# Optimization experiments

Measured on AMD Instinct MI355X. Metric: run time of the kernel, lower is better.

Reference implementation:

```python
import jax, jax.numpy as jnp
import numpy as np
import math

D, H, F = 1024, 16, 4096
DH = D // H
EPS_LN = 1e-5


def _layernorm(x, scale, bias):
    mu = jnp.mean(x, axis=-1, keepdims=True)
    var = jnp.mean(jnp.square(x - mu), axis=-1, keepdims=True)
    return (x - mu) * jax.lax.rsqrt(var + EPS_LN) * scale + bias


def setup_inputs() -> dict:
    key = jax.random.key(0)
    ks = jax.random.split(key, 16)
    B, T = 2, 2048
    src = jax.random.normal(ks[0], (B, T, D), dtype=jnp.float32)
    attn_mask = jax.random.randint(ks[1], (T, T), 0, 2) == 1  # bool [T,S], True = masked
    xavier = lambda k, shp: jax.random.uniform(k, shp, jnp.float32, -1.0, 1.0) * math.sqrt(6.0 / (shp[0] + shp[1]))
    return {
        "src": src, "attn_mask": attn_mask,
        "q_w": xavier(ks[2], (D, D)), "q_b": jnp.zeros((D,), jnp.float32),
        "k_w": xavier(ks[3], (D, D)), "k_b": jnp.zeros((D,), jnp.float32),
        "v_w": xavier(ks[4], (D, D)), "v_b": jnp.zeros((D,), jnp.float32),
        "o_w": xavier(ks[5], (D, D)), "o_b": jnp.zeros((D,), jnp.float32),
        "l1_w": xavier(ks[6], (F, D)), "l1_b": jnp.zeros((F,), jnp.float32),
        "l2_w": xavier(ks[7], (D, F)), "l2_b": jnp.zeros((D,), jnp.float32),
        "n1_s": jnp.ones((D,), jnp.float32), "n1_b": jnp.zeros((D,), jnp.float32),
        "n2_s": jnp.ones((D,), jnp.float32), "n2_b": jnp.zeros((D,), jnp.float32),
        "alpha_attn": jax.random.normal(ks[8], (), jnp.float32) * 0.1,
        "alpha_ff": jax.random.normal(ks[9], (), jnp.float32) * 0.1,
    }


def reference(src, attn_mask, q_w, q_b, k_w, k_b, v_w, v_b, o_w, o_b,
              l1_w, l1_b, l2_w, l2_b, n1_s, n1_b, n2_s, n2_b,
              alpha_attn, alpha_ff):
    B, T, _ = src.shape
    # --- self-attention block (post-norm layer, dropout=0 => identity) ---
    q = (src @ q_w.T + q_b).reshape(B, T, H, DH).transpose(0, 2, 1, 3)  # [B,H,T,DH]
    k = (src @ k_w.T + k_b).reshape(B, T, H, DH).transpose(0, 2, 1, 3)
    v = (src @ v_w.T + v_b).reshape(B, T, H, DH).transpose(0, 2, 1, 3)
    scores = jnp.einsum('bhtd,bhsd->bhts', q, k) / math.sqrt(DH)  # [B,H,T,S]
    scores = jnp.where(attn_mask[None, None, :, :], -jnp.inf, scores)
    probs = jax.nn.softmax(scores + 1e-9, axis=-1)
    probs = jnp.where(jnp.isinf(scores), 0.0, probs)  # zero where masked (custom semantics)
    attn = jnp.einsum('bhts,bhsd->bhtd', probs, v).transpose(0, 2, 1, 3).reshape(B, T, D)
    attn = attn @ o_w.T + o_b
    x = _layernorm(src + alpha_attn * attn, n1_s, n1_b)
    # --- FFN block ---
    ff = jax.nn.relu(x @ l1_w.T + l1_b) @ l2_w.T + l2_b
    x = _layernorm(x + alpha_ff * ff, n2_s, n2_b)
    return x
```

## Files before the change

### kernel.cpp

```cpp
#include <hip/hip_runtime.h>
#include <math.h>

#define Dm 1024
#define Hh 16
#define DHd 64
#define Ff 4096
#define Tt 2048
#define Bb 2

#define ATT_C2 0.18033688011112042f

typedef __bf16 bf16_8 __attribute__((ext_vector_type(8)));
typedef __bf16 bf16x2 __attribute__((ext_vector_type(2)));
typedef __bf16 bf16x4 __attribute__((ext_vector_type(4)));
typedef float  f32x4  __attribute__((ext_vector_type(4)));
typedef float  f32x16 __attribute__((ext_vector_type(16)));
typedef unsigned int u32x4 __attribute__((ext_vector_type(4)));

__device__ __forceinline__ unsigned short f2bf(float f) {
    unsigned int u = __float_as_uint(f);
    unsigned int r = (u + 0x7fffu + ((u >> 16) & 1u)) >> 16;
    return (unsigned short)r;
}

__device__ __forceinline__ bf16x2 pkbf(float a, float b) {
#if __has_builtin(__builtin_amdgcn_cvt_pk_bf16_f32)
    return __builtin_amdgcn_cvt_pk_bf16_f32(a, b);
#else
    bf16x2 r; r[0] = (__bf16)a; r[1] = (__bf16)b; return r;
#endif
}
__device__ __forceinline__ bf16x4 pkbf4(float a, float b, float c, float d) {
    bf16x2 lo = pkbf(a, b), hi = pkbf(c, d);
    return __builtin_shufflevector(lo, hi, 0, 1, 2, 3);
}

__device__ __forceinline__ void plswap32(unsigned &a, unsigned &b) {
#if __has_builtin(__builtin_amdgcn_permlane32_swap)
    auto r = __builtin_amdgcn_permlane32_swap((int)a, (int)b, false, false);
    a = (unsigned)r[0]; b = (unsigned)r[1];
#else
    asm volatile("v_permlane32_swap_b32 %0, %1" : "+v"(a), "+v"(b));
#endif
}

__device__ __forceinline__ void gld_lds16(const void* g, void* l) {
    __builtin_amdgcn_global_load_lds(
        (const __attribute__((address_space(1))) void*)g,
        (__attribute__((address_space(3))) void*)l,
        16, 0, 0);
}

__global__ __launch_bounds__(256) void preprocess_kernel(
    const float* __restrict__ q_w, const float* __restrict__ k_w,
    const float* __restrict__ v_w, const float* __restrict__ o_w,
    const float* __restrict__ l1_w, const float* __restrict__ l2_w,
    const float* __restrict__ src, const int* __restrict__ mask,
    const float* __restrict__ q_b, const float* __restrict__ k_b,
    unsigned short* __restrict__ qkw, unsigned short* __restrict__ vw16,
    unsigned short* __restrict__ ow,  unsigned short* __restrict__ l1w,
    unsigned short* __restrict__ l2w, unsigned short* __restrict__ srcb,
    unsigned* __restrict__ mbit, float* __restrict__ qkb)
{
    const int bid = blockIdx.x;
    const int tid = threadIdx.x;
    if (bid < 16384) {
        int i = bid * 256 + tid;
        const float* sp; unsigned short* dp; int off;
        if (i < 1048576) {
            if (i < 262144)      { sp = q_w; dp = qkw;           off = i; }
            else if (i < 524288) { sp = k_w; dp = qkw + 1048576; off = i - 262144; }
            else if (i < 786432) { sp = v_w; dp = vw16;          off = i - 524288; }
            else                 { sp = o_w; dp = ow;            off = i - 786432; }
        } else if (i < 2097152)  { sp = l1_w; dp = l1w;          off = i - 1048576; }
        else if (i < 3145728)    { sp = l2_w; dp = l2w;          off = i - 2097152; }
        else                     { sp = src;  dp = srcb;         off = i - 3145728; }
        float4 v = ((const float4*)sp)[off];
        ((bf16x4*)dp)[off] = pkbf4(v.x, v.y, v.z, v.w);
    } else if (bid < 16896) {
        int w = (bid - 16384) * 256 + tid;
        const int* p = mask + (size_t)w * 32;
        unsigned bits = 0;
        #pragma unroll
        for (int j = 0; j < 8; ++j) {
            int4 v = ((const int4*)p)[j];
            bits |= (v.x != 0 ? 1u : 0u) << (j * 4 + 0);
            bits |= (v.y != 0 ? 1u : 0u) << (j * 4 + 1);
            bits |= (v.z != 0 ? 1u : 0u) << (j * 4 + 2);
            bits |= (v.w != 0 ? 1u : 0u) << (j * 4 + 3);
        }
        mbit[w] = bits;
    } else {
        int i = (bid - 16896) * 256 + tid;
        qkb[i] = (i < 1024) ? q_b[i] : k_b[i - 1024];
    }
}

template<int RELU, int BF16OUT>
__global__ __launch_bounds__(256) void gemm_bf16_kernel(
    const unsigned short* __restrict__ A, const unsigned short* __restrict__ W,
    const float* __restrict__ bias, void* __restrict__ C, void* __restrict__ C2,
    int M, int N, int K, int ldc, int ksub)
{
    __shared__ __bf16 As[128][64];
    __shared__ __bf16 Bs[128][64];
    const int tid  = threadIdx.x;
    const int lane = tid & 63;
    const int wave = tid >> 6;
    const int m0 = blockIdx.y * 128;
    const int n0 = blockIdx.x * 128;
    const int lr8 = lane >> 3;
    const int gch = (lane & 7) ^ lr8;
    const int wm = (wave & 1) * 64;
    const int wn = (wave >> 1) * 64;
    const int quad = lane >> 4;
    const int lm = lane & 15;
    const int z  = blockIdx.z;
    const int kstart = z * ksub;
    void* Cz = (z == 0) ? C : C2;

    f32x4 acc[4][4];
    #pragma unroll
    for (int i = 0; i < 4; i++)
        #pragma unroll
        for (int j = 0; j < 4; j++) {
            acc[i][j][0] = 0.f; acc[i][j][1] = 0.f;
            acc[i][j][2] = 0.f; acc[i][j][3] = 0.f;
        }

    for (int k0 = kstart; k0 < kstart + ksub; k0 += 64) {
        __syncthreads();
        #pragma unroll
        for (int i = 0; i < 4; i++) {
            int seg = wave * 4 + i;
            int r = seg * 8 + lr8;
            gld_lds16(A + (size_t)(m0 + r) * K + k0 + gch * 8, &As[seg * 8][0]);
            gld_lds16(W + (size_t)(n0 + r) * K + k0 + gch * 8, &Bs[seg * 8][0]);
        }
        __syncthreads();
        #pragma unroll
        for (int kh = 0; kh < 2; kh++) {
            bf16_8 af[4], bfr[4];
            #pragma unroll
            for (int t = 0; t < 4; t++) {
                int ch = (kh * 4 + quad) ^ (lm & 7);
                af[t]  = *(const bf16_8*)&As[wm + t * 16 + lm][ch * 8];
                bfr[t] = *(const bf16_8*)&Bs[wn + t * 16 + lm][ch * 8];
            }
            #pragma unroll
            for (int i = 0; i < 4; i++)
                #pragma unroll
                for (int j = 0; j < 4; j++)
                    acc[i][j] = __builtin_amdgcn_mfma_f32_16x16x32_bf16(
                        af[i], bfr[j], acc[i][j], 0, 0, 0);
        }
    }

    float bvc[4];
    #pragma unroll
    for (int j = 0; j < 4; j++)
        bvc[j] = (z == 0) ? bias[n0 + wn + j * 16 + lm] : 0.f;

    #pragma unroll
    for (int i = 0; i < 4; i++)
        #pragma unroll
        for (int j = 0; j < 4; j++) {
            int col = n0 + wn + j * 16 + lm;
            #pragma unroll
            for (int r = 0; r < 4; r++) {
                int row = m0 + wm + i * 16 + quad * 4 + r;
                float v = acc[i][j][r] + bvc[j];
                if (RELU) v = fmaxf(v, 0.f);
                if (BF16OUT)
                    ((unsigned short*)Cz)[(size_t)row * ldc + col] = f2bf(v);
                else
                    ((float*)Cz)[(size_t)row * ldc + col] = v;
            }
        }
}

__global__ __launch_bounds__(256, 2) void gemm_ffn1_kernel(
    const unsigned short* __restrict__ A, const unsigned short* __restrict__ W,
    const float* __restrict__ bias, unsigned short* __restrict__ C)
{
    __shared__ __bf16 As[256][64];
    __shared__ __bf16 Bs[128][64];
    const int tid  = threadIdx.x;
    const int lane = tid & 63;
    const int wave = tid >> 6;
    const int m0 = blockIdx.y * 256;
    const int n0 = blockIdx.x * 128;
    const int lr8 = lane >> 3;
    const int gch = (lane & 7) ^ lr8;
    const int quad = lane >> 4;
    const int lm = lane & 15;

    f32x4 acc[4][8];
    #pragma unroll
    for (int i = 0; i < 4; i++)
        #pragma unroll
        for (int j = 0; j < 8; j++) {
            acc[i][j][0] = 0.f; acc[i][j][1] = 0.f;
            acc[i][j][2] = 0.f; acc[i][j][3] = 0.f;
        }

    for (int k0 = 0; k0 < 1024; k0 += 64) {
        __syncthreads();
        #pragma unroll
        for (int i = 0; i < 8; i++) {
            int seg = wave * 8 + i;
            int r = seg * 8 + lr8;
            gld_lds16(A + (size_t)(m0 + r) * 1024 + k0 + gch * 8, &As[seg * 8][0]);
        }
        #pragma unroll
        for (int i = 0; i < 4; i++) {
            int seg = wave * 4 + i;
            int r = seg * 8 + lr8;
            gld_lds16(W + (size_t)(n0 + r) * 1024 + k0 + gch * 8, &Bs[seg * 8][0]);
        }
        __syncthreads();
        #pragma unroll
        for (int kh = 0; kh < 2; kh++) {
            const int ch = (kh * 4 + quad) ^ (lm & 7);
            bf16_8 af[4], bfr[8];
            #pragma unroll
            for (int t = 0; t < 4; t++)
                af[t] = *(const bf16_8*)&As[wave * 64 + t * 16 + lm][ch * 8];
            #pragma unroll
            for (int j = 0; j < 8; j++)
                bfr[j] = *(const bf16_8*)&Bs[j * 16 + lm][ch * 8];
            #pragma unroll
            for (int i = 0; i < 4; i++)
                #pragma unroll
                for (int j = 0; j < 8; j++)
                    acc[i][j] = __builtin_amdgcn_mfma_f32_16x16x32_bf16(
                        af[i], bfr[j], acc[i][j], 0, 0, 0);
        }
    }

    float bv[8];
    #pragma unroll
    for (int j = 0; j < 8; j++) bv[j] = bias[n0 + j * 16 + lm];

    #pragma unroll
    for (int i = 0; i < 4; i++)
        #pragma unroll
        for (int j = 0; j < 8; j++) {
            int col = n0 + j * 16 + lm;
            #pragma unroll
            for (int r = 0; r < 4; r++) {
                int row = m0 + wave * 64 + i * 16 + quad * 4 + r;
                float v = fmaxf(acc[i][j][r] + bv[j], 0.f);
                C[(size_t)row * Ff + col] = f2bf(v);
            }
        }
}

__global__ __launch_bounds__(256) void gemm_qkvt_kernel(
    const unsigned short* __restrict__ srcb, const unsigned short* __restrict__ qkw,
    const unsigned short* __restrict__ vw16, const float* __restrict__ qkb,
    const float* __restrict__ v_b,
    unsigned short* __restrict__ qk16, unsigned short* __restrict__ vtf)
{
    const int bid = blockIdx.x;
    const unsigned short *A, *W;
    const float* bias;
    unsigned short* C;
    int m0, n0, ldc;
    bool qscale, rowbias;
    if (bid < 512) {
        A = srcb; W = qkw; bias = qkb; C = qk16;
        n0 = (bid & 15) * 128; m0 = (bid >> 4) * 128;
        ldc = 2048; qscale = true; rowbias = false;
    } else {
        int b2 = bid - 512;
        A = vw16; W = srcb; bias = v_b; C = vtf;
        n0 = (b2 & 31) * 128; m0 = (b2 >> 5) * 128;
        ldc = 4096; qscale = false; rowbias = true;
    }
    const int K = 1024;

    __shared__ __bf16 As[128][64];
    __shared__ __bf16 Bs[128][64];
    const int tid  = threadIdx.x;
    const int lane = tid & 63;
    const int wave = tid >> 6;
    const int lr8 = lane >> 3;
    const int gch = (lane & 7) ^ lr8;
    const int wm = (wave & 1) * 64;
    const int wn = (wave >> 1) * 64;
    const int quad = lane >> 4;
    const int lm = lane & 15;

    f32x4 acc[4][4];
    #pragma unroll
    for (int i = 0; i < 4; i++)
        #pragma unroll
        for (int j = 0; j < 4; j++) {
            acc[i][j][0] = 0.f; acc[i][j][1] = 0.f;
            acc[i][j][2] = 0.f; acc[i][j][3] = 0.f;
        }

    for (int k0 = 0; k0 < K; k0 += 64) {
        __syncthreads();
        #pragma unroll
        for (int i = 0; i < 4; i++) {
            int seg = wave * 4 + i;
            int r = seg * 8 + lr8;
            gld_lds16(A + (size_t)(m0 + r) * K + k0 + gch * 8, &As[seg * 8][0]);
            gld_lds16(W + (size_t)(n0 + r) * K + k0 + gch * 8, &Bs[seg * 8][0]);
        }
        __syncthreads();
        #pragma unroll
        for (int kh = 0; kh < 2; kh++) {
            bf16_8 af[4], bfr[4];
            #pragma unroll
            for (int t = 0; t < 4; t++) {
                int ch = (kh * 4 + quad) ^ (lm & 7);
                af[t]  = *(const bf16_8*)&As[wm + t * 16 + lm][ch * 8];
                bfr[t] = *(const bf16_8*)&Bs[wn + t * 16 + lm][ch * 8];
            }
            #pragma unroll
            for (int i = 0; i < 4; i++)
                #pragma unroll
                for (int j = 0; j < 4; j++)
                    acc[i][j] = __builtin_amdgcn_mfma_f32_16x16x32_bf16(
                        af[i], bfr[j], acc[i][j], 0, 0, 0);
        }
    }

    float bvc[4];
    float brr[4][4];
    if (!rowbias) {
        #pragma unroll
        for (int j = 0; j < 4; j++) bvc[j] = bias[n0 + wn + j * 16 + lm];
    } else {
        #pragma unroll
        for (int i = 0; i < 4; i++) {
            float4 t4 = *(const float4*)&bias[m0 + wm + i * 16 + quad * 4];
            brr[i][0] = t4.x; brr[i][1] = t4.y; brr[i][2] = t4.z; brr[i][3] = t4.w;
        }
    }

    #pragma unroll
    for (int i = 0; i < 4; i++)
        #pragma unroll
        for (int j = 0; j < 4; j++) {
            int col = n0 + wn + j * 16 + lm;
            #pragma unroll
            for (int r = 0; r < 4; r++) {
                int row = m0 + wm + i * 16 + quad * 4 + r;
                float v = acc[i][j][r] + (rowbias ? brr[i][r] : bvc[j]);
                if (qscale && col < 1024) v *= ATT_C2;
                C[(size_t)row * ldc + col] = f2bf(v);
            }
        }
}

__global__ __launch_bounds__(256) void attn_mfma_kernel(
    const unsigned short* __restrict__ qk,
    const unsigned short* __restrict__ vt,
    const unsigned* __restrict__ mb,
    unsigned short* __restrict__ out)
{
    __shared__ __bf16 Ks[2][128 * 64];
    __shared__ __bf16 Vt[2][64 * 128];
    __shared__ float  l_s[128];

    const int tid  = threadIdx.x;
    const int lane = tid & 63;
    const int wave = tid >> 6;
    const int l31  = lane & 31;
    const int hi   = lane >> 5;
    const int x7   = l31 & 7;
    const int bh = blockIdx.y;
    const int b = bh >> 4, h = bh & 15;
    const int tw = blockIdx.x * 128 + wave * 32;

    bf16_8 qf[4];
    #pragma unroll
    for (int ds4 = 0; ds4 < 4; ++ds4)
        qf[ds4] = *(const bf16_8*)(qk +
            (size_t)(b * Tt + tw + l31) * 2048 + h * DHd + ds4 * 16 + hi * 8);

    f32x16 oacc[2];
    #pragma unroll
    for (int d = 0; d < 2; ++d)
        #pragma unroll
        for (int r = 0; r < 16; ++r) oacc[d][r] = 0.f;
    float lsum = 0.f;

    const int krow8 = lane >> 3;
    const int kj    = (lane & 7) ^ krow8;
    const int vr4   = lane >> 4;

    auto STAGE = [&](int nb, int s0) {
        #pragma unroll
        for (int i = 0; i < 4; ++i) {
            int ci = wave * 4 + i;
            {
                int r = 8 * ci + krow8;
                const unsigned short* g = qk +
                    (size_t)(b * Tt + s0 + r) * 2048 + 1024 + h * DHd + kj * 8;
                gld_lds16(g, &Ks[nb][ci * 512]);
            }
            {
                int d = 4 * ci + vr4;
                int jj = (lane & 15) ^ (d & 7);
                const unsigned short* g = vt +
                    (size_t)(h * DHd + d) * 4096 + b * Tt + s0 + jj * 8;
                gld_lds16(g, &Vt[nb][ci * 512]);
            }
        }
    };

    STAGE(0, 0);

    for (int st = 0; st < 16; ++st) {
        const int cb = st & 1;
        const int s0 = st * 128;
        __syncthreads();

        unsigned mwv[4];
        #pragma unroll
        for (int sb = 0; sb < 4; ++sb)
            mwv[sb] = mb[(size_t)(tw + l31) * 64 + (s0 >> 5) + sb];

        if (st < 15) STAGE(cb ^ 1, s0 + 128);

        #pragma unroll
        for (int sb = 0; sb < 4; ++sb) {
            f32x16 sacc;
            #pragma unroll
            for (int r = 0; r < 16; ++r) sacc[r] = 0.f;
            #pragma unroll
            for (int ds4 = 0; ds4 < 4; ++ds4) {
                bf16_8 kf = *(const bf16_8*)&Ks[cb][
                    (sb * 32 + l31) * 64 + (((ds4 * 2 + hi) ^ x7) * 8)];
                sacc = __builtin_amdgcn_mfma_f32_32x32x16_bf16(
                    kf, qf[ds4], sacc, 0, 0, 0);
            }
            const unsigned mword = mwv[sb];
            float p[16];
            #pragma unroll
            for (int g = 0; g < 4; ++g)
                #pragma unroll
                for (int m = 0; m < 4; ++m) {
                    const int reg = g * 4 + m;
                    const int srow = m + 8 * g + 4 * hi;
                    float x = ((mword >> srow) & 1u) ? -1e30f : sacc[reg];
                    float e = __builtin_amdgcn_exp2f(x);
                    p[reg] = e;
                    lsum += e;
                }
            unsigned u[4], v[4];
            #pragma unroll
            for (int g = 0; g < 4; ++g) {
                u[g] = __builtin_bit_cast(unsigned, pkbf(p[g * 4 + 0], p[g * 4 + 1]));
                v[g] = __builtin_bit_cast(unsigned, pkbf(p[g * 4 + 2], p[g * 4 + 3]));
            }
            plswap32(u[0], u[1]); plswap32(v[0], v[1]);
            plswap32(u[2], u[3]); plswap32(v[2], v[3]);
            u32x4 w0; w0[0] = u[0]; w0[1] = v[0]; w0[2] = u[1]; w0[3] = v[1];
            u32x4 w1; w1[0] = u[2]; w1[1] = v[2]; w1[2] = u[3]; w1[3] = v[3];
            bf16_8 pa0 = __builtin_bit_cast(bf16_8, w0);
            bf16_8 pa1 = __builtin_bit_cast(bf16_8, w1);
            #pragma unroll
            for (int kst = 0; kst < 2; ++kst) {
                bf16_8 pa = kst ? pa1 : pa0;
                #pragma unroll
                for (int dblk = 0; dblk < 2; ++dblk) {
                    int cpos = (sb * 4 + kst * 2 + hi) ^ x7;
                    bf16_8 vf = *(const bf16_8*)&Vt[cb][
                        ((dblk * 32 + l31) * 16 + cpos) * 8];
                    oacc[dblk] = __builtin_amdgcn_mfma_f32_32x32x16_bf16(
                        pa, vf, oacc[dblk], 0, 0, 0);
                }
            }
        }
    }

    unsigned la = __builtin_bit_cast(unsigned, lsum), lb = la;
    plswap32(la, lb);
    float ltot = __builtin_bit_cast(float, la) + __builtin_bit_cast(float, lb);
    l_s[wave * 32 + l31] = (ltot > 0.f) ? 1.f / ltot : 0.f;
    __syncthreads();

    #pragma unroll
    for (int g = 0; g < 4; ++g)
        #pragma unroll
        for (int m = 0; m < 4; ++m) {
            const int reg = g * 4 + m;
            const int tr = m + 8 * g + 4 * hi;
            float inv = l_s[wave * 32 + tr];
            int row = b * Tt + tw + tr;
            #pragma unroll
            for (int dblk = 0; dblk < 2; ++dblk)
                out[(size_t)row * Dm + h * DHd + dblk * 32 + l31] =
                    f2bf(oacc[dblk][reg] * inv);
        }
}

template<int NPARTS, int BASEBF, int OUTF32, int OUTBF>
__global__ __launch_bounds__(256) void residual_ln_kernel(
    const void* __restrict__ base, const float* __restrict__ d0,
    const float* __restrict__ d1,
    const float* __restrict__ alpha_p, const float* __restrict__ scale,
    const float* __restrict__ bias, float* __restrict__ out,
    unsigned short* __restrict__ out_bf)
{
    const int row = blockIdx.x;
    const int tid = threadIdx.x;
    const float alpha = alpha_p[0];
    float4 xb;
    if (BASEBF) {
        bf16x4 bb = ((const bf16x4*)((const unsigned short*)base + (size_t)row * Dm))[tid];
        xb.x = (float)bb[0]; xb.y = (float)bb[1]; xb.z = (float)bb[2]; xb.w = (float)bb[3];
    } else {
        xb = ((const float4*)((const float*)base + (size_t)row * Dm))[tid];
    }
    float4 xd = ((const float4*)(d0 + (size_t)row * Dm))[tid];
    if (NPARTS == 2) {
        float4 x2 = ((const float4*)(d1 + (size_t)row * Dm))[tid];
        xd.x += x2.x; xd.y += x2.y; xd.z += x2.z; xd.w += x2.w;
    }
    float4 x;
    x.x = xb.x + alpha * xd.x;
    x.y = xb.y + alpha * xd.y;
    x.z = xb.z + alpha * xd.z;
    x.w = xb.w + alpha * xd.w;
    float s  = x.x + x.y + x.z + x.w;
    float sq = x.x*x.x + x.y*x.y + x.z*x.z + x.w*x.w;
    #pragma unroll
    for (int off = 32; off > 0; off >>= 1) {
        s  += __shfl_down(s, off, 64);
        sq += __shfl_down(sq, off, 64);
    }
    __shared__ float red[8];
    const int w = tid >> 6;
    if ((tid & 63) == 0) { red[w] = s; red[4 + w] = sq; }
    __syncthreads();
    s  = red[0] + red[1] + red[2] + red[3];
    sq = red[4] + red[5] + red[6] + red[7];
    const float mu  = s * (1.f / Dm);
    const float var = sq * (1.f / Dm) - mu * mu;
    const float r   = rsqrtf(var + 1e-5f);
    float4 sc = ((const float4*)scale)[tid];
    float4 bi = ((const float4*)bias)[tid];
    float4 o;
    o.x = (x.x - mu) * r * sc.x + bi.x;
    o.y = (x.y - mu) * r * sc.y + bi.y;
    o.z = (x.z - mu) * r * sc.z + bi.z;
    o.w = (x.w - mu) * r * sc.w + bi.w;
    if (OUTF32)
        ((float4*)(out + (size_t)row * Dm))[tid] = o;
    if (OUTBF)
        ((bf16x4*)(out_bf + (size_t)row * Dm))[tid] = pkbf4(o.x, o.y, o.z, o.w);
}

extern "C" void kernel_launch(void* const* d_in, const int* in_sizes, int n_in,
                              void* d_out, int out_size, void* d_ws, size_t ws_size,
                              hipStream_t stream)
{
    (void)in_sizes; (void)n_in; (void)out_size; (void)ws_size;
    const float* src  = (const float*)d_in[0];
    const int*   mask = (const int*)  d_in[1];
    const float* q_w  = (const float*)d_in[2];
    const float* q_b  = (const float*)d_in[3];
    const float* k_w  = (const float*)d_in[4];
    const float* k_b  = (const float*)d_in[5];
    const float* v_w  = (const float*)d_in[6];
    const float* v_b  = (const float*)d_in[7];
    const float* o_w  = (const float*)d_in[8];
    const float* o_b  = (const float*)d_in[9];
    const float* l1_w = (const float*)d_in[10];
    const float* l1_b = (const float*)d_in[11];
    const float* l2_w = (const float*)d_in[12];
    const float* l2_b = (const float*)d_in[13];
    const float* n1_s = (const float*)d_in[14];
    const float* n1_b = (const float*)d_in[15];
    const float* n2_s = (const float*)d_in[16];
    const float* n2_b = (const float*)d_in[17];
    const float* a_attn = (const float*)d_in[18];
    const float* a_ff   = (const float*)d_in[19];

    const size_t MB = 1024 * 1024;
    char* w = (char*)d_ws;
    unsigned short* qkw  = (unsigned short*)(w + 0);
    unsigned short* vw16 = (unsigned short*)(w + 4  * MB);
    unsigned short* ow   = (unsigned short*)(w + 6  * MB);
    unsigned short* l1w  = (unsigned short*)(w + 8  * MB);
    unsigned short* l2w  = (unsigned short*)(w + 16 * MB);
    unsigned short* srcb = (unsigned short*)(w + 24 * MB);
    unsigned short* qk16 = (unsigned short*)(w + 32 * MB);
    unsigned short* vtf  = (unsigned short*)(w + 48 * MB);
    unsigned*       mbit = (unsigned*)      (w + 56 * MB);
    float*          qkb  = (float*)         (w + 56 * MB + 524288);
    unsigned short* atb  = (unsigned short*)(w + 24 * MB);
    float*          o0   = (float*)         (w + 58 * MB);
    float*          o1   = (float*)         (w + 74 * MB);
    unsigned short* x1b  = (unsigned short*)(w + 48 * MB);
    unsigned short* hb   = (unsigned short*)(w + 58 * MB);
    float*          fp0  = (float*)         (w + 0);
    float*          fp1  = (float*)         (w + 32 * MB);

    const int MR = Bb * Tt;
    dim3 blk(256);

    preprocess_kernel<<<dim3(16904), blk, 0, stream>>>(
        q_w, k_w, v_w, o_w, l1_w, l2_w, src, mask, q_b, k_b,
        qkw, vw16, ow, l1w, l2w, srcb, mbit, qkb);
    gemm_qkvt_kernel<<<dim3(768), blk, 0, stream>>>(
        srcb, qkw, vw16, qkb, v_b, qk16, vtf);
    attn_mfma_kernel<<<dim3(16, 32), blk, 0, stream>>>(qk16, vtf, mbit, atb);
    gemm_bf16_kernel<0, 0><<<dim3(8, 32, 2), blk, 0, stream>>>(
        atb, ow, o_b, o0, o1, MR, Dm, Dm, Dm, 512);
    residual_ln_kernel<2, 0, 0, 1><<<dim3(MR), blk, 0, stream>>>(
        src, o0, o1, a_attn, n1_s, n1_b, nullptr, x1b);
    gemm_ffn1_kernel<<<dim3(32, 16), blk, 0, stream>>>(x1b, l1w, l1_b, hb);
    gemm_bf16_kernel<0, 0><<<dim3(8, 32, 2), blk, 0, stream>>>(
        hb, l2w, l2_b, fp0, fp1, MR, Dm, Ff, Dm, Ff / 2);
    residual_ln_kernel<2, 1, 1, 0><<<dim3(MR), blk, 0, stream>>>(
        x1b, fp0, fp1, a_ff, n2_s, n2_b, (float*)d_out, nullptr);
}
```

Measured before the change: 370.3 us.

## Transpose mask bits for scalar loads and compute row sums via MFMA

The mask bitmap is re-laid out so that each 32-query block stores one 32-bit word per key column. The attention kernel can then fetch a wave's mask with scalar s_load_dwordx8 and apply it through v_cndmask using a 64-bit SGPR lane mask. The per-lane exp-sum, the permlane swap and the LDS reduction are replaced by an extra MFMA of P against a ones vector, which accumulates the row sums directly in the output layout. The cost is one more MFMA per key block, plus inline asm with an explicit lgkmcnt wait that may stall. The preprocess mask loads also become strided column reads.

Result: no change. 376.9 us (+1.8%).

```diff
diff --git a/kernel.cpp b/kernel.cpp
--- a/kernel.cpp
+++ b/kernel.cpp
@@ -16,6 +16,7 @@
 typedef float  f32x4  __attribute__((ext_vector_type(4)));
 typedef float  f32x16 __attribute__((ext_vector_type(16)));
 typedef unsigned int u32x4 __attribute__((ext_vector_type(4)));
+typedef unsigned int u32x8s __attribute__((ext_vector_type(8)));
 
 __device__ __forceinline__ unsigned short f2bf(float f) {
     unsigned int u = __float_as_uint(f);
@@ -49,6 +50,24 @@
         (const __attribute__((address_space(1))) void*)g,
         (__attribute__((address_space(3))) void*)l,
         16, 0, 0);
+}
+
+__device__ __forceinline__ void sload32(const unsigned* p,
+        u32x8s &a, u32x8s &b, u32x8s &c, u32x8s &d) {
+    asm volatile(
+        "s_load_dwordx8 %0, %4, 0x0\n\t"
+        "s_load_dwordx8 %1, %4, 0x20\n\t"
+        "s_load_dwordx8 %2, %4, 0x40\n\t"
+        "s_load_dwordx8 %3, %4, 0x60\n\t"
+        "s_waitcnt lgkmcnt(0)"
+        : "=s"(a), "=s"(b), "=s"(c), "=s"(d)
+        : "s"(p));
+}
+
+__device__ __forceinline__ float selkeep(float e, unsigned long long keep) {
+    float r;
+    asm("v_cndmask_b32 %0, 0, %1, %2" : "=v"(r) : "v"(e), "s"(keep));
+    return r;
 }
 
 __global__ __launch_bounds__(256) void preprocess_kernel(
@@ -60,7 +79,7 @@
     unsigned short* __restrict__ qkw, unsigned short* __restrict__ vw16,
     unsigned short* __restrict__ ow,  unsigned short* __restrict__ l1w,
     unsigned short* __restrict__ l2w, unsigned short* __restrict__ srcb,
-    unsigned* __restrict__ mbit, float* __restrict__ qkb)
+    unsigned* __restrict__ mbT, float* __restrict__ qkb)
 {
     const int bid = blockIdx.x;
     const int tid = threadIdx.x;
@@ -79,17 +98,13 @@
         ((bf16x4*)dp)[off] = pkbf4(v.x, v.y, v.z, v.w);
     } else if (bid < 16896) {
         int w = (bid - 16384) * 256 + tid;
-        const int* p = mask + (size_t)w * 32;
+        int tw32 = w >> 11, s = w & 2047;
+        const int* p = mask + (size_t)(tw32 * 32) * 2048 + s;
         unsigned bits = 0;
         #pragma unroll
-        for (int j = 0; j < 8; ++j) {
-            int4 v = ((const int4*)p)[j];
-            bits |= (v.x != 0 ? 1u : 0u) << (j * 4 + 0);
-            bits |= (v.y != 0 ? 1u : 0u) << (j * 4 + 1);
-            bits |= (v.z != 0 ? 1u : 0u) << (j * 4 + 2);
-            bits |= (v.w != 0 ? 1u : 0u) << (j * 4 + 3);
-        }
-        mbit[w] = bits;
+        for (int j = 0; j < 32; ++j)
+            bits |= (p[(size_t)j * 2048] == 0 ? 1u : 0u) << j;
+        mbT[w] = bits;
     } else {
         int i = (bid - 16896) * 256 + tid;
         qkb[i] = (i < 1024) ? q_b[i] : k_b[i - 1024];
@@ -360,12 +375,11 @@
 __global__ __launch_bounds__(256) void attn_mfma_kernel(
     const unsigned short* __restrict__ qk,
     const unsigned short* __restrict__ vt,
-    const unsigned* __restrict__ mb,
+    const unsigned* __restrict__ mbT,
     unsigned short* __restrict__ out)
 {
     __shared__ __bf16 Ks[2][128 * 64];
     __shared__ __bf16 Vt[2][64 * 128];
-    __shared__ float  l_s[128];
 
     const int tid  = threadIdx.x;
     const int lane = tid & 63;
@@ -376,6 +390,8 @@
     const int bh = blockIdx.y;
     const int b = bh >> 4, h = bh & 15;
     const int tw = blockIdx.x * 128 + wave * 32;
+    const int wvu = __builtin_amdgcn_readfirstlane(wave);
+    const unsigned* mrow = mbT + (size_t)(blockIdx.x * 4 + wvu) * 2048;
 
     bf16_8 qf[4];
     #pragma unroll
@@ -384,11 +400,18 @@
             (size_t)(b * Tt + tw + l31) * 2048 + h * DHd + ds4 * 16 + hi * 8);
 
     f32x16 oacc[2];
-    #pragma unroll
-    for (int d = 0; d < 2; ++d)
-        #pragma unroll
-        for (int r = 0; r < 16; ++r) oacc[d][r] = 0.f;
-    float lsum = 0.f;
+    f32x16 ol;
+    f32x16 z16;
+    #pragma unroll
+    for (int r = 0; r < 16; ++r) {
+        oacc[0][r] = 0.f; oacc[1][r] = 0.f; ol[r] = 0.f; z16[r] = 0.f;
+    }
+    bf16_8 vone;
+    {
+        __bf16 one = (__bf16)1.0f;
+        #pragma unroll
+        for (int j = 0; j < 8; ++j) vone[j] = one;
+    }
 
     const int krow8 = lane >> 3;
     const int kj    = (lane & 7) ^ krow8;
@@ -421,18 +444,14 @@
         const int s0 = st * 128;
         __syncthreads();
 
-        unsigned mwv[4];
-        #pragma unroll
-        for (int sb = 0; sb < 4; ++sb)
-            mwv[sb] = mb[(size_t)(tw + l31) * 64 + (s0 >> 5) + sb];
-
         if (st < 15) STAGE(cb ^ 1, s0 + 128);
 
         #pragma unroll
         for (int sb = 0; sb < 4; ++sb) {
-            f32x16 sacc;
-            #pragma unroll
-            for (int r = 0; r < 16; ++r) sacc[r] = 0.f;
+            u32x8s ma, mbw, mc, md;
+            sload32(mrow + s0 + sb * 32, ma, mbw, mc, md);
+
+            f32x16 sacc = z16;
             #pragma unroll
             for (int ds4 = 0; ds4 < 4; ++ds4) {
                 bf16_8 kf = *(const bf16_8*)&Ks[cb][
@@ -440,19 +459,20 @@
                 sacc = __builtin_amdgcn_mfma_f32_32x32x16_bf16(
                     kf, qf[ds4], sacc, 0, 0, 0);
             }
-            const unsigned mword = mwv[sb];
             float p[16];
             #pragma unroll
-            for (int g = 0; g < 4; ++g)
+            for (int g = 0; g < 4; ++g) {
+                u32x8s vv = (g == 0) ? ma : (g == 1) ? mbw : (g == 2) ? mc : md;
                 #pragma unroll
                 for (int m = 0; m < 4; ++m) {
                     const int reg = g * 4 + m;
-                    const int srow = m + 8 * g + 4 * hi;
-                    float x = ((mword >> srow) & 1u) ? -1e30f : sacc[reg];
-                    float e = __builtin_amdgcn_exp2f(x);
-                    p[reg] = e;
-                    lsum += e;
+                    unsigned long long keep =
+                        ((unsigned long long)vv[m + 4] << 32) |
+                        (unsigned long long)vv[m];
+                    float e = __builtin_amdgcn_exp2f(sacc[reg]);
+                    p[reg] = selkeep(e, keep);
                 }
+            }
             unsigned u[4], v[4];
             #pragma unroll
             for (int g = 0; g < 4; ++g) {
@@ -476,15 +496,11 @@
                     oacc[dblk] = __builtin_amdgcn_mfma_f32_32x32x16_bf16(
                         pa, vf, oacc[dblk], 0, 0, 0);
                 }
-            }
-        }
-    }
-
-    unsigned la = __builtin_bit_cast(unsigned, lsum), lb = la;
-    plswap32(la, lb);
-    float ltot = __builtin_bit_cast(float, la) + __builtin_bit_cast(float, lb);
-    l_s[wave * 32 + l31] = (ltot > 0.f) ? 1.f / ltot : 0.f;
-    __syncthreads();
+                ol = __builtin_amdgcn_mfma_f32_32x32x16_bf16(
+                    pa, vone, ol, 0, 0, 0);
+            }
+        }
+    }
 
     #pragma unroll
     for (int g = 0; g < 4; ++g)
@@ -492,7 +508,8 @@
         for (int m = 0; m < 4; ++m) {
             const int reg = g * 4 + m;
             const int tr = m + 8 * g + 4 * hi;
-            float inv = l_s[wave * 32 + tr];
+            float l = ol[reg];
+            float inv = (l > 0.f) ? 1.f / l : 0.f;
             int row = b * Tt + tw + tr;
             #pragma unroll
             for (int dblk = 0; dblk < 2; ++dblk)
@@ -594,7 +611,7 @@
     unsigned short* srcb = (unsigned short*)(w + 24 * MB);
     unsigned short* qk16 = (unsigned short*)(w + 32 * MB);
     unsigned short* vtf  = (unsigned short*)(w + 48 * MB);
-    unsigned*       mbit = (unsigned*)      (w + 56 * MB);
+    unsigned*       mbT  = (unsigned*)      (w + 56 * MB);
     float*          qkb  = (float*)         (w + 56 * MB + 524288);
     unsigned short* atb  = (unsigned short*)(w + 24 * MB);
     float*          o0   = (float*)         (w + 58 * MB);
@@ -609,10 +626,10 @@
 
     preprocess_kernel<<<dim3(16904), blk, 0, stream>>>(
         q_w, k_w, v_w, o_w, l1_w, l2_w, src, mask, q_b, k_b,
-        qkw, vw16, ow, l1w, l2w, srcb, mbit, qkb);
+        qkw, vw16, ow, l1w, l2w, srcb, mbT, qkb);
     gemm_qkvt_kernel<<<dim3(768), blk, 0, stream>>>(
         srcb, qkw, vw16, qkb, v_b, qk16, vtf);
-    attn_mfma_kernel<<<dim3(16, 32), blk, 0, stream>>>(qk16, vtf, mbit, atb);
+    attn_mfma_kernel<<<dim3(16, 32), blk, 0, stream>>>(qk16, vtf, mbT, atb);
     gemm_bf16_kernel<0, 0><<<dim3(8, 32, 2), blk, 0, stream>>>(
         atb, ow, o_b, o0, o1, MR, Dm, Dm, Dm, 512);
     residual_ln_kernel<2, 0, 0, 1><<<dim3(MR), blk, 0, stream>>>(
```
